# Performance work log

Measured on AMD Instinct MI355X. Metric: run time of the kernel, lower is better.

The kernel has to match this reference:

```python
import jax, jax.numpy as jnp
import numpy as np

STEPLIM = 20   # module steplim; loop runs while iter <= steplim -> steplim+1 iterations
TOL = 1e-4     # early-stopping tolerance on change in mean NN error


def _nn1(pc1, pc2):
    """1-NN of each point in pc1 [B,N,3] within pc2 [B,M,3] under L2 norm.
    Uses the GEMM form ||a||^2 + ||b||^2 - 2 a.b instead of materializing the
    [B,N,M,3] broadcasted difference tensor. Returns (min_dist [B,N], idx [B,N])."""
    d2 = (jnp.sum(pc1 * pc1, axis=-1)[..., :, None]
          + jnp.sum(pc2 * pc2, axis=-1)[..., None, :]
          - 2.0 * jnp.einsum('bnd,bmd->bnm', pc1, pc2))
    d2 = jnp.maximum(d2, 1e-12)                  # clamp FP cancellation negatives
    idx = jnp.argmin(d2, axis=-1)                # [B, N]
    dmin = jnp.sqrt(jnp.take_along_axis(d2, idx[..., None], axis=-1)[..., 0])
    return dmin, idx


def _kabsch(src, dst):
    """Rigid transform (R, t) minimizing ||R@src + t - dst|| via SVD (EPnP._points_transform)."""
    c1 = jnp.mean(src, axis=-2, keepdims=True)   # [B,1,3]
    c2 = jnp.mean(dst, axis=-2, keepdims=True)
    H = jnp.einsum('bni,bnj->bij', src - c1, dst - c2)          # [B,3,3]
    U, S, Vt = jnp.linalg.svd(H, full_matrices=False)
    det = jnp.linalg.det(jnp.einsum('bki,bjk->bij', Vt, U))     # det(V U^T)
    d = jnp.sign(det)
    D = jnp.stack([jnp.ones_like(d), jnp.ones_like(d), d], axis=-1)  # reflection fix
    R = jnp.einsum('bki,bk,bjk->bij', Vt, D, U)                 # V diag(1,1,d) U^T
    t = c2[..., 0, :] - jnp.einsum('bij,bj->bi', R, c1[..., 0, :])
    return R, t


def _icp(p1, p2):
    B = p1.shape[0]

    def step(carry, _):
        pc, err, done = carry
        dmin, idx = _nn1(pc, p2)
        # errnew = sum(sum(values)/len(values)): mean over batch of per-point sums
        errnew = jnp.sum(dmin) / B
        # source quirk: uses the LAST batch element's indices for all batches
        matched = p2[:, idx[-1], :]                              # [B,N,3]
        R, t = _kabsch(pc, matched)
        pc_new = jnp.einsum('bij,bnj->bni', R, pc) + t[:, None, :]
        # torch loop updates temppc BEFORE the break check, then freezes
        pc_out = jnp.where(done, pc, pc_new)
        err_out = jnp.where(done, err, errnew)
        done_out = done | (jnp.abs(err - errnew) < TOL)
        return (pc_out, err_out, done_out), None

    init = (p1, jnp.asarray(0.0, p1.dtype), jnp.asarray(False))
    (pc, _, _), _ = jax.lax.scan(step, init, None, length=STEPLIM + 1)
    R, t = _kabsch(p1, pc)
    return jnp.concatenate([R, t[..., None]], axis=-1)           # [B,3,4] = [R | t]


def setup_inputs() -> dict:
    key = jax.random.key(0)
    k1, k2 = jax.random.split(key)
    p1 = jax.random.normal(k1, (1, 8192, 3), dtype=jnp.float32)
    p2 = jax.random.normal(k2, (1, 8192, 3), dtype=jnp.float32)
    return {"p1": p1, "p2": p2}


def reference(p1, p2):
    return _icp(p1, p2)
```

## Files before the change

kernel.cpp:

```cpp
#include <hip/hip_runtime.h>
#include <math.h>

#define N_PTS 8192
#define ICP_STEPS 21
#define ICP_TOL 1e-4

#define NBLK 256
#define BSIZE 1024
#define QPW 8
#define NSETS 16

struct IcpCtl {
  double err;
  double Rc[9];
  double tc[3];
  int done;
};

__global__ __launch_bounds__(256) void icp_prep(const float* __restrict__ p2,
                                                float4* __restrict__ p2aug,
                                                IcpCtl* __restrict__ ctl,
                                                double* __restrict__ acc,
                                                unsigned* __restrict__ gtick,
                                                unsigned* __restrict__ root) {
  int t = blockIdx.x * 256 + threadIdx.x;
  float x = p2[3*t], y = p2[3*t+1], z = p2[3*t+2];
  p2aug[t] = make_float4(x, y, z, fmaf(x, x, fmaf(y, y, z*z)));
  if (t < NSETS * 16) acc[t] = 0.0;
  if (t < NSETS) gtick[t << 4] = 0u;
  if (t == 0) {
    *root = 0u;
    ctl->err = 0.0; ctl->done = 0;
    #pragma unroll
    for (int i = 0; i < 9; ++i) ctl->Rc[i] = (i % 4 == 0) ? 1.0 : 0.0;
    ctl->tc[0] = ctl->tc[1] = ctl->tc[2] = 0.0;
  }
}

__device__ __forceinline__ void kabsch_solve(const double* s, double* R, double* T) {
  const double n = (double)N_PTS;
  const double c1x = s[1]/n, c1y = s[2]/n, c1z = s[3]/n;
  const double c2x = s[4]/n, c2y = s[5]/n, c2z = s[6]/n;
  const double h00 = s[7]  - n*c1x*c2x, h01 = s[8]  - n*c1x*c2y, h02 = s[9]  - n*c1x*c2z;
  const double h10 = s[10] - n*c1y*c2x, h11 = s[11] - n*c1y*c2y, h12 = s[12] - n*c1y*c2z;
  const double h20 = s[13] - n*c1z*c2x, h21 = s[14] - n*c1z*c2y, h22 = s[15] - n*c1z*c2z;

  double a00 = h00*h00 + h10*h10 + h20*h20;
  double a01 = h00*h01 + h10*h11 + h20*h21;
  double a02 = h00*h02 + h10*h12 + h20*h22;
  double a11 = h01*h01 + h11*h11 + h21*h21;
  double a12 = h01*h02 + h11*h12 + h21*h22;
  double a22 = h02*h02 + h12*h12 + h22*h22;

  double v00=1.0, v01=0.0, v02=0.0;
  double v10=0.0, v11=1.0, v12=0.0;
  double v20=0.0, v21=0.0, v22=1.0;

#define ROT3(app, aqq, apq, arp, arq, vpa, vqa, vpb, vqb, vpc, vqc)              \
  {                                                                              \
    double apq_ = apq;                                                           \
    if (fabs(apq_) > 1e-300) {                                                   \
      double tau = (aqq - app) / (2.0 * apq_);                                   \
      double tt  = (tau >= 0.0 ? 1.0 : -1.0) / (fabs(tau) + sqrt(1.0 + tau*tau));\
      double c_  = 1.0 / sqrt(1.0 + tt*tt), sn = tt * c_;                        \
      app -= tt * apq_;  aqq += tt * apq_;  apq = 0.0;                           \
      double t1 = arp, t2 = arq;                                                 \
      arp = c_*t1 - sn*t2;  arq = sn*t1 + c_*t2;                                 \
      t1 = vpa; t2 = vqa; vpa = c_*t1 - sn*t2; vqa = sn*t1 + c_*t2;              \
      t1 = vpb; t2 = vqb; vpb = c_*t1 - sn*t2; vqb = sn*t1 + c_*t2;              \
      t1 = vpc; t2 = vqc; vpc = c_*t1 - sn*t2; vqc = sn*t1 + c_*t2;              \
    }                                                                            \
  }

  #pragma unroll
  for (int sweep = 0; sweep < 6; ++sweep) {
    ROT3(a00, a11, a01, a02, a12, v00, v01, v10, v11, v20, v21);
    ROT3(a00, a22, a02, a01, a12, v00, v02, v10, v12, v20, v22);
    ROT3(a11, a22, a12, a01, a02, v01, v02, v11, v12, v21, v22);
  }
#undef ROT3

  double l0 = a00, l1 = a11, l2 = a22;
  double e0x=v00, e0y=v10, e0z=v20;
  double e1x=v01, e1y=v11, e1z=v21;
  double e2x=v02, e2y=v12, e2z=v22;
#define CSWAP(la, lb, xa, ya, za, xb, yb, zb)                                    \
  if (lb > la) { double t_;                                                      \
    t_ = la; la = lb; lb = t_;  t_ = xa; xa = xb; xb = t_;                       \
    t_ = ya; ya = yb; yb = t_;  t_ = za; za = zb; zb = t_; }
  CSWAP(l0, l1, e0x, e0y, e0z, e1x, e1y, e1z);
  CSWAP(l0, l2, e0x, e0y, e0z, e2x, e2y, e2z);
  CSWAP(l1, l2, e1x, e1y, e1z, e2x, e2y, e2z);
#undef CSWAP

  double detV = e0x*(e1y*e2z - e1z*e2y) - e0y*(e1x*e2z - e1z*e2x)
              + e0z*(e1x*e2y - e1y*e2x);
  const double dsg = (detV >= 0.0) ? 1.0 : -1.0;

  double u0x = h00*e0x + h01*e0y + h02*e0z;
  double u0y = h10*e0x + h11*e0y + h12*e0z;
  double u0z = h20*e0x + h21*e0y + h22*e0z;
  double n0 = sqrt(u0x*u0x + u0y*u0y + u0z*u0z);
  if (!(n0 > 1e-150)) {
    R[0]=1.0; R[1]=0.0; R[2]=0.0; R[3]=0.0; R[4]=1.0; R[5]=0.0;
    R[6]=0.0; R[7]=0.0; R[8]=1.0;
    T[0]=c2x-c1x; T[1]=c2y-c1y; T[2]=c2z-c1z;
    return;
  }
  u0x /= n0; u0y /= n0; u0z /= n0;
  double u1x = h00*e1x + h01*e1y + h02*e1z;
  double u1y = h10*e1x + h11*e1y + h12*e1z;
  double u1z = h20*e1x + h21*e1y + h22*e1z;
  const double d10 = u1x*u0x + u1y*u0y + u1z*u0z;
  u1x -= d10*u0x; u1y -= d10*u0y; u1z -= d10*u0z;
  double n1 = sqrt(u1x*u1x + u1y*u1y + u1z*u1z);
  if (!(n1 > 1e-150)) {
    R[0]=1.0; R[1]=0.0; R[2]=0.0; R[3]=0.0; R[4]=1.0; R[5]=0.0;
    R[6]=0.0; R[7]=0.0; R[8]=1.0;
    T[0]=c2x-c1x; T[1]=c2y-c1y; T[2]=c2z-c1z;
    return;
  }
  u1x /= n1; u1y /= n1; u1z /= n1;
  const double u2x = u0y*u1z - u0z*u1y;
  const double u2y = u0z*u1x - u0x*u1z;
  const double u2z = u0x*u1y - u0y*u1x;

  R[0] = e0x*u0x + e1x*u1x + dsg*e2x*u2x;
  R[1] = e0x*u0y + e1x*u1y + dsg*e2x*u2y;
  R[2] = e0x*u0z + e1x*u1z + dsg*e2x*u2z;
  R[3] = e0y*u0x + e1y*u1x + dsg*e2y*u2x;
  R[4] = e0y*u0y + e1y*u1y + dsg*e2y*u2y;
  R[5] = e0y*u0z + e1y*u1z + dsg*e2y*u2z;
  R[6] = e0z*u0x + e1z*u1x + dsg*e2z*u2x;
  R[7] = e0z*u0y + e1z*u1y + dsg*e2z*u2y;
  R[8] = e0z*u0z + e1z*u1z + dsg*e2z*u2z;
  T[0] = c2x - (R[0]*c1x + R[1]*c1y + R[2]*c1z);
  T[1] = c2y - (R[3]*c1x + R[4]*c1y + R[5]*c1z);
  T[2] = c2z - (R[6]*c1x + R[7]*c1y + R[8]*c1z);
}

__global__ __launch_bounds__(BSIZE) void icp_step(const float* __restrict__ p1,
                                                  const float4* __restrict__ p2aug,
                                                  IcpCtl* __restrict__ ctl,
                                                  double* __restrict__ acc,
                                                  unsigned* __restrict__ gtick,
                                                  unsigned* __restrict__ root,
                                                  float* __restrict__ out) {
  if (ctl->done) return;
  __shared__ float4 cand[N_PTS];
  __shared__ unsigned long long pkbuf[32][4];
  __shared__ float4 qlds[32];
  __shared__ double pairbuf[32][17];
  __shared__ double setbuf[16][17];
  __shared__ double totbuf[16];
  __shared__ int solverFlag;

  const int tid  = threadIdx.x;
  const int lane = tid & 63;
  const int w    = tid >> 6;
  const int g    = w >> 2;
  const int s    = w & 3;
  const int bid  = blockIdx.x;

  if (tid == 0) solverFlag = 0;

  #pragma unroll
  for (int k = 0; k < 8; ++k) {
    const int i = (k << 10) + tid;
    cand[i] = p2aug[i];
  }

  const double R0 = ctl->Rc[0], R1 = ctl->Rc[1], R2 = ctl->Rc[2];
  const double R3 = ctl->Rc[3], R4 = ctl->Rc[4], R5 = ctl->Rc[5];
  const double R6 = ctl->Rc[6], R7 = ctl->Rc[7], R8 = ctl->Rc[8];
  const double T0 = ctl->tc[0], T1 = ctl->tc[1], T2 = ctl->tc[2];

  const int qbase = (bid << 5) + (g << 3);
  float axv[QPW], ayv[QPW], azv[QPW], best[QPW];
  int bidx[QPW];
  float qxr[QPW], qyr[QPW], qzr[QPW];
  #pragma unroll
  for (int j = 0; j < QPW; ++j) {
    const int q = qbase + j;
    const double X = (double)p1[3*q], Y = (double)p1[3*q+1], Z = (double)p1[3*q+2];
    qxr[j] = (float)(R0*X + R1*Y + R2*Z + T0);
    qyr[j] = (float)(R3*X + R4*Y + R5*Z + T1);
    qzr[j] = (float)(R6*X + R7*Y + R8*Z + T2);
    axv[j] = -2.f*qxr[j]; ayv[j] = -2.f*qyr[j]; azv[j] = -2.f*qzr[j];
    best[j] = __builtin_inff(); bidx[j] = 0;
  }
  if (s == 0 && lane == 0) {
    #pragma unroll
    for (int j = 0; j < QPW; ++j)
      qlds[(g << 3) + j] = make_float4(qxr[j], qyr[j], qzr[j], 0.f);
  }
  __syncthreads();

  const int cb = s << 11;
  #pragma unroll 8
  for (int kk = 0; kk < 32; ++kk) {
    const int cidx = cb + (kk << 6) + lane;
    float4 c = cand[cidx];
    #pragma unroll
    for (int j = 0; j < QPW; ++j) {
      float d = fmaf(axv[j], c.x, fmaf(ayv[j], c.y, fmaf(azv[j], c.z, c.w)));
      if (d < best[j]) { best[j] = d; bidx[j] = cidx; }
    }
  }

  unsigned long long pk[QPW];
  #pragma unroll
  for (int j = 0; j < QPW; ++j) {
    unsigned u = __float_as_uint(best[j]);
    u ^= (unsigned)((int)u >> 31) | 0x80000000u;
    pk[j] = ((unsigned long long)u << 32) | (unsigned)bidx[j];
  }
  #pragma unroll
  for (int j = 0; j < QPW; ++j) {
    #pragma unroll
    for (int o = 1; o < 64; o <<= 1) {
      unsigned long long other = __shfl_xor(pk[j], o, 64);
      pk[j] = (other < pk[j]) ? other : pk[j];
    }
  }
  if (lane == 0) {
    #pragma unroll
    for (int j = 0; j < QPW; ++j)
      pkbuf[(g << 3) + j][s] = pk[j];
  }
  __syncthreads();

  if (tid < 32) {
    unsigned long long m = pkbuf[tid][0];
    unsigned long long m1 = pkbuf[tid][1]; m = (m1 < m) ? m1 : m;
    unsigned long long m2 = pkbuf[tid][2]; m = (m2 < m) ? m2 : m;
    unsigned long long m3 = pkbuf[tid][3]; m = (m3 < m) ? m3 : m;
    const unsigned idx = (unsigned)(m & 0xffffffffull);
    const float4 q4 = qlds[tid];
    const float4 b4 = cand[idx];
    const double ax = q4.x, ay = q4.y, az = q4.z;
    const double bx = b4.x, by = b4.y, bz = b4.z;
    const double d2 = (ax*ax + ay*ay + az*az) + (bx*bx + by*by + bz*bz)
                    - 2.0*(ax*bx + ay*by + az*bz);
    pairbuf[tid][0]  = sqrt(fmax(d2, 1e-12));
    pairbuf[tid][1]  = ax;    pairbuf[tid][2]  = ay;    pairbuf[tid][3]  = az;
    pairbuf[tid][4]  = bx;    pairbuf[tid][5]  = by;    pairbuf[tid][6]  = bz;
    pairbuf[tid][7]  = ax*bx; pairbuf[tid][8]  = ax*by; pairbuf[tid][9]  = ax*bz;
    pairbuf[tid][10] = ay*bx; pairbuf[tid][11] = ay*by; pairbuf[tid][12] = ay*bz;
    pairbuf[tid][13] = az*bx; pairbuf[tid][14] = az*by; pairbuf[tid][15] = az*bz;
  }
  __syncthreads();

  if (tid < 16) {
    double ssum = 0.0;
    #pragma unroll
    for (int i = 0; i < 32; ++i) ssum += pairbuf[i][tid];
    atomicAdd(acc + ((bid & 15) << 4) + tid, ssum);
  }
  if (tid == 0) {
    asm volatile("s_waitcnt vmcnt(0)" ::: "memory");
    const int gi = bid & 15;
    unsigned og = atomicAdd(gtick + (gi << 4), 1u);
    if (og == 15u) {
      unsigned orr = atomicAdd(root, 1u);
      if (orr == 15u) solverFlag = 1;
    }
  }
  __syncthreads();
  if (!solverFlag) return;

  double val = 0.0;
  if (tid < 256) val = atomicAdd(acc + tid, 0.0);
  if (tid < 256) setbuf[tid >> 4][tid & 15] = val;
  __syncthreads();
  if (tid < 16) {
    double t2 = 0.0;
    #pragma unroll
    for (int i = 0; i < 16; ++i) t2 += setbuf[i][tid];
    totbuf[tid] = t2;
  }
  __syncthreads();

  if (tid == 0) {
    double sm[16];
    #pragma unroll
    for (int i = 0; i < 16; ++i) sm[i] = totbuf[i];
    double R[9], T[3];
    kabsch_solve(sm, R, T);
    double Rc[9] = {R0,R1,R2,R3,R4,R5,R6,R7,R8};
    double tc[3] = {T0,T1,T2};
    double Rn[9], tn[3];
    #pragma unroll
    for (int i = 0; i < 3; ++i) {
      #pragma unroll
      for (int j = 0; j < 3; ++j)
        Rn[3*i+j] = R[3*i+0]*Rc[0+j] + R[3*i+1]*Rc[3+j] + R[3*i+2]*Rc[6+j];
      tn[i] = R[3*i+0]*tc[0] + R[3*i+1]*tc[1] + R[3*i+2]*tc[2] + T[i];
    }
    #pragma unroll
    for (int i = 0; i < 9; ++i) ctl->Rc[i] = Rn[i];
    #pragma unroll
    for (int i = 0; i < 3; ++i) ctl->tc[i] = tn[i];
    const double errnew = sm[0];
    ctl->done = (fabs(ctl->err - errnew) < ICP_TOL) ? 1 : 0;
    ctl->err  = errnew;
    #pragma unroll
    for (int i = 0; i < 3; ++i) {
      out[4*i + 0] = (float)Rn[3*i + 0];
      out[4*i + 1] = (float)Rn[3*i + 1];
      out[4*i + 2] = (float)Rn[3*i + 2];
      out[4*i + 3] = (float)tn[i];
    }
    *root = 0u;
  }
  if (tid < 256) acc[tid] = 0.0;
  if (tid < 16) gtick[tid << 4] = 0u;
}

extern "C" void kernel_launch(void* const* d_in, const int* in_sizes, int n_in,
                              void* d_out, int out_size, void* d_ws, size_t ws_size,
                              hipStream_t stream) {
  const float* p1 = (const float*)d_in[0];
  const float* p2 = (const float*)d_in[1];
  float* out = (float*)d_out;

  char* ws = (char*)d_ws;
  float4* p2aug  = (float4*)ws;
  IcpCtl* ctl    = (IcpCtl*)(ws + 128*1024);
  double* acc    = (double*)(ws + 132*1024);
  unsigned* gtick = (unsigned*)(ws + 136*1024);
  unsigned* root  = (unsigned*)(ws + 140*1024);

  icp_prep<<<N_PTS/256, 256, 0, stream>>>(p2, p2aug, ctl, acc, gtick, root);
  for (int it = 0; it < ICP_STEPS; ++it)
    icp_step<<<NBLK, BSIZE, 0, stream>>>(p1, p2aug, ctl, acc, gtick, root, out);
}
```

Before: 496.6 us.

## Halve block size and stream candidates through LDS in two chunks

Changes the NN kernel from 1024-thread blocks with the full 8192-point candidate set in LDS to 512-thread blocks that load candidates in two 4096-point chunks. Each wave now owns 4 queries and scans all candidates itself, so the cross-wave min merge is removed. The point is to cut LDS use per block (128KB to 64KB) and shrink blocks, which could allow more concurrent blocks per CU. In exchange it adds a sync per chunk, gives each wave a longer serial scan, and reads the matched point from global memory.

Measured after the change: 478.3 us (median of 2 runs). -3.7%, faster.

```diff
diff --git a/kernel.cpp b/kernel.cpp
--- a/kernel.cpp
+++ b/kernel.cpp
@@ -6,8 +6,10 @@
 #define ICP_TOL 1e-4
 
 #define NBLK 256
-#define BSIZE 1024
-#define QPW 8
+#define BSIZE 512
+#define QPW 4
+#define CH 4096
+#define NCH 2
 #define NSETS 16
 
 struct IcpCtl {
@@ -147,8 +149,8 @@
                                                   unsigned* __restrict__ root,
                                                   float* __restrict__ out) {
   if (ctl->done) return;
-  __shared__ float4 cand[N_PTS];
-  __shared__ unsigned long long pkbuf[32][4];
+  __shared__ float4 cand[CH];
+  __shared__ unsigned long long pkbuf[8][5];
   __shared__ float4 qlds[32];
   __shared__ double pairbuf[32][17];
   __shared__ double setbuf[16][17];
@@ -158,54 +160,47 @@
   const int tid  = threadIdx.x;
   const int lane = tid & 63;
   const int w    = tid >> 6;
-  const int g    = w >> 2;
-  const int s    = w & 3;
   const int bid  = blockIdx.x;
 
   if (tid == 0) solverFlag = 0;
-
-  #pragma unroll
-  for (int k = 0; k < 8; ++k) {
-    const int i = (k << 10) + tid;
-    cand[i] = p2aug[i];
-  }
 
   const double R0 = ctl->Rc[0], R1 = ctl->Rc[1], R2 = ctl->Rc[2];
   const double R3 = ctl->Rc[3], R4 = ctl->Rc[4], R5 = ctl->Rc[5];
   const double R6 = ctl->Rc[6], R7 = ctl->Rc[7], R8 = ctl->Rc[8];
   const double T0 = ctl->tc[0], T1 = ctl->tc[1], T2 = ctl->tc[2];
 
-  const int qbase = (bid << 5) + (g << 3);
+  const int qb = (bid << 5) + (w << 2);
   float axv[QPW], ayv[QPW], azv[QPW], best[QPW];
   int bidx[QPW];
-  float qxr[QPW], qyr[QPW], qzr[QPW];
   #pragma unroll
   for (int j = 0; j < QPW; ++j) {
-    const int q = qbase + j;
+    const int q = qb + j;
     const double X = (double)p1[3*q], Y = (double)p1[3*q+1], Z = (double)p1[3*q+2];
-    qxr[j] = (float)(R0*X + R1*Y + R2*Z + T0);
-    qyr[j] = (float)(R3*X + R4*Y + R5*Z + T1);
-    qzr[j] = (float)(R6*X + R7*Y + R8*Z + T2);
-    axv[j] = -2.f*qxr[j]; ayv[j] = -2.f*qyr[j]; azv[j] = -2.f*qzr[j];
+    const float qx = (float)(R0*X + R1*Y + R2*Z + T0);
+    const float qy = (float)(R3*X + R4*Y + R5*Z + T1);
+    const float qz = (float)(R6*X + R7*Y + R8*Z + T2);
+    axv[j] = -2.f*qx; ayv[j] = -2.f*qy; azv[j] = -2.f*qz;
     best[j] = __builtin_inff(); bidx[j] = 0;
-  }
-  if (s == 0 && lane == 0) {
-    #pragma unroll
-    for (int j = 0; j < QPW; ++j)
-      qlds[(g << 3) + j] = make_float4(qxr[j], qyr[j], qzr[j], 0.f);
-  }
-  __syncthreads();
-
-  const int cb = s << 11;
-  #pragma unroll 8
-  for (int kk = 0; kk < 32; ++kk) {
-    const int cidx = cb + (kk << 6) + lane;
-    float4 c = cand[cidx];
-    #pragma unroll
-    for (int j = 0; j < QPW; ++j) {
-      float d = fmaf(axv[j], c.x, fmaf(ayv[j], c.y, fmaf(azv[j], c.z, c.w)));
-      if (d < best[j]) { best[j] = d; bidx[j] = cidx; }
-    }
+    if (lane == 0) qlds[(w << 2) + j] = make_float4(qx, qy, qz, 0.f);
+  }
+
+  for (int cb = 0; cb < NCH; ++cb) {
+    const int cbase = cb << 12;
+    #pragma unroll
+    for (int kk = 0; kk < 8; ++kk)
+      cand[(kk << 9) + tid] = p2aug[cbase + (kk << 9) + tid];
+    __syncthreads();
+    #pragma unroll 4
+    for (int kk = 0; kk < 64; ++kk) {
+      const int cidx = cbase + (kk << 6) + lane;
+      float4 c = cand[(kk << 6) + lane];
+      #pragma unroll
+      for (int j = 0; j < QPW; ++j) {
+        float d = fmaf(axv[j], c.x, fmaf(ayv[j], c.y, fmaf(azv[j], c.z, c.w)));
+        if (d < best[j]) { best[j] = d; bidx[j] = cidx; }
+      }
+    }
+    __syncthreads();
   }
 
   unsigned long long pk[QPW];
@@ -225,19 +220,15 @@
   }
   if (lane == 0) {
     #pragma unroll
-    for (int j = 0; j < QPW; ++j)
-      pkbuf[(g << 3) + j][s] = pk[j];
+    for (int j = 0; j < QPW; ++j) pkbuf[w][j] = pk[j];
   }
   __syncthreads();
 
   if (tid < 32) {
-    unsigned long long m = pkbuf[tid][0];
-    unsigned long long m1 = pkbuf[tid][1]; m = (m1 < m) ? m1 : m;
-    unsigned long long m2 = pkbuf[tid][2]; m = (m2 < m) ? m2 : m;
-    unsigned long long m3 = pkbuf[tid][3]; m = (m3 < m) ? m3 : m;
+    const unsigned long long m = pkbuf[tid >> 2][tid & 3];
     const unsigned idx = (unsigned)(m & 0xffffffffull);
     const float4 q4 = qlds[tid];
-    const float4 b4 = cand[idx];
+    const float4 b4 = p2aug[idx];
     const double ax = q4.x, ay = q4.y, az = q4.z;
     const double bx = b4.x, by = b4.y, bz = b4.z;
     const double d2 = (ax*ax + ay*ay + az*az) + (bx*bx + by*by + bz*bz)
```
